# Kernel tuning notes

Hardware: AMD Instinct MI355X
Metric: run time of the kernel (lower is better)

Reference implementation:

```python
import jax, jax.numpy as jnp
import numpy as np

D_MODEL = 1024
D_INNER = 2048   # d_model * expansion_factor(2)
D_CONV = 4
N_EXPERTS = 8
TOP_K = 2


def setup_inputs() -> dict:
    key = jax.random.key(0)
    ks = jax.random.split(key, 6)
    s = 0.02
    return {
        "x": jax.random.normal(ks[0], (4, 2048, D_MODEL), jnp.float32),
        "Wr": jax.random.normal(ks[1], (N_EXPERTS, D_MODEL), jnp.float32) * s,
        "br": jnp.zeros((N_EXPERTS,), jnp.float32),
        "Win": jax.random.normal(ks[2], (N_EXPERTS, 2 * D_INNER, D_MODEL), jnp.float32) * s,
        "conv_w": jax.random.normal(ks[3], (N_EXPERTS, D_INNER, D_CONV), jnp.float32) * s,
        "conv_b": jnp.zeros((N_EXPERTS, D_INNER), jnp.float32),
        "Dp": jnp.ones((N_EXPERTS, D_INNER), jnp.float32),
        "Wout": jax.random.normal(ks[4], (N_EXPERTS, D_MODEL, D_INNER), jnp.float32) * s,
    }


def reference(x, Wr, br, Win, conv_w, conv_b, Dp, Wout):
    B, L, C = x.shape
    xf = x.reshape(-1, C)                                   # [N, C]
    logits = xf @ Wr.T + br                                 # [N, E]
    probs = jax.nn.softmax(logits.astype(jnp.float32), axis=-1)
    tw, ti = jax.lax.top_k(probs, TOP_K)                    # [N, k]
    tw = tw / jnp.sum(tw, axis=-1, keepdims=True)
    oh = jax.nn.one_hot(ti, N_EXPERTS, dtype=jnp.float32)   # [N, k, E]
    load = oh.sum(1).mean(0)                                # [E]
    aux_loss = jnp.sum(load * load)
    # per-token combine weight for each expert (sum over top-k slots)
    cw = jnp.einsum('nk,nke->ne', tw, oh)                   # [N, E]
    out = jnp.zeros_like(xf)
    for j in range(N_EXPERTS):
        # Per-token expert (L=1 inside the original loop): causal depthwise
        # conv with left padding reduces to last-tap * x + bias.
        xz = xf @ Win[j].T                                  # [N, 2*D_INNER]
        xi, z = xz[:, :D_INNER], xz[:, D_INNER:]
        xa = jax.nn.silu(xi * conv_w[j, :, -1] + conv_b[j])
        y = xa * Dp[j] * jax.nn.silu(z)
        out = out + cw[:, j:j + 1].astype(xf.dtype) * (y @ Wout[j].T)
    return out.reshape(B, L, C), aux_loss
```

## Files before the change

### kernel.cpp

```cpp
#include <hip/hip_runtime.h>
#include <hip/hip_bf16.h>
#include <stdint.h>

#define NTOK 8192
#define CDIM 1024
#define DIN  2048
#define NEXP 8
#define NSLOT (NTOK * 2)

typedef __bf16 bf16x8 __attribute__((ext_vector_type(8)));
typedef float  f32x4  __attribute__((ext_vector_type(4)));

typedef __attribute__((address_space(1))) const unsigned char GBUF;
typedef __attribute__((address_space(3))) unsigned char LBUF;

__device__ __forceinline__ void gload_lds16(const void* g, void* l) {
    __builtin_amdgcn_global_load_lds((GBUF*)g, (LBUF*)l, 16, 0, 0);
}

__device__ __forceinline__ ushort f2bf(float f) {
    union { float f; unsigned u; } v; v.f = f;
    unsigned u = v.u;
    u += 0x7fffu + ((u >> 16) & 1u);
    return (ushort)(u >> 16);
}
__device__ __forceinline__ float bf2f(ushort u) {
    union { float f; unsigned u; } v; v.u = ((unsigned)u) << 16; return v.f;
}
__device__ __forceinline__ float silu_f(float x) { return x / (1.f + __expf(-x)); }

__device__ __forceinline__ bf16x8 lds_swz(const ushort* L, int row, int kof) {
    return *(const bf16x8*)&L[row * 64 + ((((kof >> 3) ^ row) & 7) << 3)];
}

__global__ void __launch_bounds__(256) k_cvt(const float* __restrict__ src,
                                             ushort* __restrict__ dst, int n4) {
    int i = blockIdx.x * 256 + threadIdx.x;
    int stride = gridDim.x * 256;
    for (; i < n4; i += stride) {
        float4 v = ((const float4*)src)[i];
        ushort4 o;
        o.x = f2bf(v.x); o.y = f2bf(v.y); o.z = f2bf(v.z); o.w = f2bf(v.w);
        ((ushort4*)dst)[i] = o;
    }
}

__global__ void __launch_bounds__(256) k_router(
    const float* __restrict__ x, const float* __restrict__ Wr,
    const float* __restrict__ br, int* __restrict__ counts,
    int* __restrict__ tok_e, float* __restrict__ tok_w,
    ushort* __restrict__ xb) {
    int wave = blockIdx.x * 4 + (threadIdx.x >> 6);
    int lane = threadIdx.x & 63;
    const float4* row = (const float4*)(x + (size_t)wave * CDIM);
    ushort4* xrow = (ushort4*)(xb + (size_t)wave * CDIM);
    float acc[NEXP];
#pragma unroll
    for (int e = 0; e < NEXP; ++e) acc[e] = 0.f;
#pragma unroll
    for (int j = 0; j < 4; ++j) {
        float4 v = row[j * 64 + lane];
        ushort4 o;
        o.x = f2bf(v.x); o.y = f2bf(v.y); o.z = f2bf(v.z); o.w = f2bf(v.w);
        xrow[j * 64 + lane] = o;
#pragma unroll
        for (int e = 0; e < NEXP; ++e) {
            float4 w = ((const float4*)(Wr + e * CDIM))[j * 64 + lane];
            acc[e] += v.x * w.x + v.y * w.y + v.z * w.z + v.w * w.w;
        }
    }
#pragma unroll
    for (int off = 32; off > 0; off >>= 1)
#pragma unroll
        for (int e = 0; e < NEXP; ++e) acc[e] += __shfl_xor(acc[e], off, 64);
    if (lane == 0) {
        float l[NEXP];
#pragma unroll
        for (int e = 0; e < NEXP; ++e) l[e] = acc[e] + br[e];
        int i0 = 0; float l0 = l[0];
#pragma unroll
        for (int e = 1; e < NEXP; ++e) if (l[e] > l0) { l0 = l[e]; i0 = e; }
        int i1 = -1; float l1 = -1e30f;
#pragma unroll
        for (int e = 0; e < NEXP; ++e) if (e != i0 && l[e] > l1) { l1 = l[e]; i1 = e; }
        float s  = __expf(l1 - l0);
        float w0 = 1.f / (1.f + s);
        float w1 = 1.f - w0;
        tok_e[wave * 2] = i0; tok_e[wave * 2 + 1] = i1;
        tok_w[wave * 2] = w0; tok_w[wave * 2 + 1] = w1;
        atomicAdd(&counts[i0], 1); atomicAdd(&counts[i1], 1);
    }
}

__global__ void k_scan(const int* __restrict__ counts, int* __restrict__ offsets,
                       float* __restrict__ out_aux) {
    if (threadIdx.x == 0 && blockIdx.x == 0) {
        int o = 0;
        for (int e = 0; e < NEXP; ++e) { offsets[e] = o; o += counts[e]; }
        offsets[NEXP] = o;
        float aux = 0.f;
        for (int e = 0; e < NEXP; ++e) {
            float ld = (float)counts[e] * (1.f / (float)NTOK);
            aux += ld * ld;
        }
        *out_aux = aux;
    }
}

__global__ void __launch_bounds__(256) k_scatter(
    const int* __restrict__ tok_e, const float* __restrict__ tok_w,
    const int* __restrict__ offsets, int* __restrict__ cursor,
    int* __restrict__ perm_token, int* __restrict__ tok_slot) {
    int t = blockIdx.x * 256 + threadIdx.x;
    if (t >= NTOK) return;
#pragma unroll
    for (int k = 0; k < 2; ++k) {
        int e = tok_e[t * 2 + k];
        int pos = atomicAdd(&cursor[e], 1);
        int s = offsets[e] + pos;
        perm_token[s] = t;
        tok_slot[t * 2 + k] = s;
    }
}

__global__ void __launch_bounds__(512, 2) k_gemm1(
    const ushort* __restrict__ xb, const ushort* __restrict__ Winb,
    const float* __restrict__ conv_w, const float* __restrict__ conv_b,
    const float* __restrict__ Dp, const int* __restrict__ counts,
    const int* __restrict__ offsets, const int* __restrict__ perm_token,
    ushort* __restrict__ y) {
    int h = blockIdx.x;
    int vb = (h & 7) * 160 + (h >> 3);
    int e   = vb / 160;
    int r   = vb % 160;
    int mt0 = r >> 4;
    int nt  = r & 15;
    int cnt = counts[e];
    if (cnt == 0) return;
    int base = offsets[e];
    int mtiles = (cnt + 255) >> 8;
    int n0 = nt * 128;

    __shared__ ushort aL[2][256 * 64];
    __shared__ ushort bL[2][256 * 64];

    int tid = threadIdx.x, lane = tid & 63, w = tid >> 6;
    int Mw = w >> 1, Nw = w & 1;
    const ushort* WinE = Winb + (size_t)e * (2 * DIN) * CDIM;
    int schunk = ((tid & 7) ^ ((tid >> 3) & 7)) << 3;

    uint bsrc[4];
#pragma unroll
    for (int i = 0; i < 4; ++i) {
        int rr = i * 64 + (tid >> 3);
        int grow = (rr < 128) ? (n0 + rr) : (DIN + n0 + (rr - 128));
        bsrc[i] = (uint)grow * CDIM + schunk;
    }

#define STAGE1(bi, kk0) do { \
        gload_lds16(xb   + asrc[0] + (kk0), &aL[bi][(0 * 512 + tid) * 8]); \
        gload_lds16(xb   + asrc[1] + (kk0), &aL[bi][(1 * 512 + tid) * 8]); \
        gload_lds16(xb   + asrc[2] + (kk0), &aL[bi][(2 * 512 + tid) * 8]); \
        gload_lds16(xb   + asrc[3] + (kk0), &aL[bi][(3 * 512 + tid) * 8]); \
        gload_lds16(WinE + bsrc[0] + (kk0), &bL[bi][(0 * 512 + tid) * 8]); \
        gload_lds16(WinE + bsrc[1] + (kk0), &bL[bi][(1 * 512 + tid) * 8]); \
        gload_lds16(WinE + bsrc[2] + (kk0), &bL[bi][(2 * 512 + tid) * 8]); \
        gload_lds16(WinE + bsrc[3] + (kk0), &bL[bi][(3 * 512 + tid) * 8]); \
    } while (0)

    for (int mt = mt0; mt < mtiles; mt += 10) {
        int rem = cnt - mt * 256;
        uint asrc[4];
#pragma unroll
        for (int i = 0; i < 4; ++i) {
            int rr = i * 64 + (tid >> 3);
            int sidx = base + mt * 256 + (rr < rem ? rr : 0);
            asrc[i] = (uint)perm_token[sidx] * CDIM + schunk;
        }

        f32x4 accXi[4][4], accZ[4][4];
#pragma unroll
        for (int m = 0; m < 4; ++m)
#pragma unroll
            for (int n = 0; n < 4; ++n) {
                accXi[m][n] = f32x4{0.f, 0.f, 0.f, 0.f};
                accZ[m][n]  = f32x4{0.f, 0.f, 0.f, 0.f};
            }

        STAGE1(0, 0);
        __syncthreads();
#pragma unroll 2
        for (int kt = 0; kt < 16; ++kt) {
            int cur = kt & 1;
            if (kt < 15) STAGE1(cur ^ 1, (kt + 1) * 64);
            const ushort* A = &aL[cur][0];
            const ushort* B = &bL[cur][0];
#pragma unroll
            for (int kk = 0; kk < 64; kk += 32) {
                int kof = kk + (lane >> 4) * 8;
                bf16x8 af[4], bxi[4], bz[4];
#pragma unroll
                for (int m = 0; m < 4; ++m)
                    af[m] = lds_swz(A, Mw * 64 + m * 16 + (lane & 15), kof);
#pragma unroll
                for (int n = 0; n < 4; ++n) {
                    int cl = Nw * 64 + n * 16 + (lane & 15);
                    bxi[n] = lds_swz(B, cl, kof);
                    bz[n]  = lds_swz(B, 128 + cl, kof);
                }
#pragma unroll
                for (int m = 0; m < 4; ++m)
#pragma unroll
                    for (int n = 0; n < 4; ++n) {
                        accXi[m][n] = __builtin_amdgcn_mfma_f32_16x16x32_bf16(af[m], bxi[n], accXi[m][n], 0, 0, 0);
                        accZ[m][n]  = __builtin_amdgcn_mfma_f32_16x16x32_bf16(af[m], bz[n],  accZ[m][n],  0, 0, 0);
                    }
            }
            __syncthreads();
        }
#pragma unroll
        for (int n = 0; n < 4; ++n) {
            int c = n0 + Nw * 64 + n * 16 + (lane & 15);
            float cwl = conv_w[((size_t)e * DIN + c) * 4 + 3];
            float cb  = conv_b[(size_t)e * DIN + c];
            float dp  = Dp[(size_t)e * DIN + c];
#pragma unroll
            for (int m = 0; m < 4; ++m)
#pragma unroll
                for (int q = 0; q < 4; ++q) {
                    int rl = Mw * 64 + m * 16 + (lane >> 4) * 4 + q;
                    if (rl < rem) {
                        int slot = base + mt * 256 + rl;
                        float xi = accXi[m][n][q], z = accZ[m][n][q];
                        float yv = silu_f(xi * cwl + cb) * dp * silu_f(z);
                        y[(size_t)slot * DIN + c] = f2bf(yv);
                    }
                }
        }
    }
#undef STAGE1
}

__global__ void __launch_bounds__(512, 2) k_gemm2(
    const ushort* __restrict__ y, const ushort* __restrict__ Woutb,
    const int* __restrict__ counts, const int* __restrict__ offsets,
    ushort* __restrict__ so) {
    int h = blockIdx.x;
    int vb = (h & 7) * 80 + (h >> 3);
    int e   = vb / 80;
    int r   = vb % 80;
    int mt0 = r >> 3;
    int nt  = r & 7;
    int cnt = counts[e];
    if (cnt == 0) return;
    int base = offsets[e];
    int mtiles = (cnt + 255) >> 8;
    int c0 = nt * 128;

    __shared__ ushort aL[2][256 * 64];
    __shared__ ushort bL[2][128 * 64];

    int tid = threadIdx.x, lane = tid & 63, w = tid >> 6;
    int Mw = w >> 1, Nw = w & 1;
    const ushort* WoutE = Woutb + (size_t)e * CDIM * DIN;
    int schunk = ((tid & 7) ^ ((tid >> 3) & 7)) << 3;

    uint bsrc[2];
#pragma unroll
    for (int i = 0; i < 2; ++i) {
        int rr = i * 64 + (tid >> 3);
        bsrc[i] = (uint)(c0 + rr) * DIN + schunk;
    }

#define STAGE2(bi, kk0) do { \
        gload_lds16(y     + asrc[0] + (kk0), &aL[bi][(0 * 512 + tid) * 8]); \
        gload_lds16(y     + asrc[1] + (kk0), &aL[bi][(1 * 512 + tid) * 8]); \
        gload_lds16(y     + asrc[2] + (kk0), &aL[bi][(2 * 512 + tid) * 8]); \
        gload_lds16(y     + asrc[3] + (kk0), &aL[bi][(3 * 512 + tid) * 8]); \
        gload_lds16(WoutE + bsrc[0] + (kk0), &bL[bi][(0 * 512 + tid) * 8]); \
        gload_lds16(WoutE + bsrc[1] + (kk0), &bL[bi][(1 * 512 + tid) * 8]); \
    } while (0)

    for (int mt = mt0; mt < mtiles; mt += 10) {
        int rem = cnt - mt * 256;
        uint asrc[4];
#pragma unroll
        for (int i = 0; i < 4; ++i) {
            int rr = i * 64 + (tid >> 3);
            int slot = base + mt * 256 + (rr < rem ? rr : 0);
            asrc[i] = (uint)slot * DIN + schunk;
        }
        f32x4 acc[4][4];
#pragma unroll
        for (int m = 0; m < 4; ++m)
#pragma unroll
            for (int n = 0; n < 4; ++n) acc[m][n] = f32x4{0.f, 0.f, 0.f, 0.f};

        STAGE2(0, 0);
        __syncthreads();
#pragma unroll 2
        for (int kt = 0; kt < 32; ++kt) {
            int cur = kt & 1;
            if (kt < 31) STAGE2(cur ^ 1, (kt + 1) * 64);
            const ushort* A = &aL[cur][0];
            const ushort* B = &bL[cur][0];
#pragma unroll
            for (int kk = 0; kk < 64; kk += 32) {
                int kof = kk + (lane >> 4) * 8;
                bf16x8 af[4], bfr[4];
#pragma unroll
                for (int m = 0; m < 4; ++m)
                    af[m] = lds_swz(A, Mw * 64 + m * 16 + (lane & 15), kof);
#pragma unroll
                for (int n = 0; n < 4; ++n)
                    bfr[n] = lds_swz(B, Nw * 64 + n * 16 + (lane & 15), kof);
#pragma unroll
                for (int m = 0; m < 4; ++m)
#pragma unroll
                    for (int n = 0; n < 4; ++n)
                        acc[m][n] = __builtin_amdgcn_mfma_f32_16x16x32_bf16(af[m], bfr[n], acc[m][n], 0, 0, 0);
            }
            __syncthreads();
        }
#pragma unroll
        for (int m = 0; m < 4; ++m)
#pragma unroll
            for (int q = 0; q < 4; ++q) {
                int rl = Mw * 64 + m * 16 + (lane >> 4) * 4 + q;
                if (rl < rem) {
                    int slot = base + mt * 256 + rl;
#pragma unroll
                    for (int n = 0; n < 4; ++n) {
                        int col = c0 + Nw * 64 + n * 16 + (lane & 15);
                        so[(size_t)slot * CDIM + col] = f2bf(acc[m][n][q]);
                    }
                }
            }
    }
#undef STAGE2
}

__global__ void __launch_bounds__(256) k_combine(
    const ushort* __restrict__ so, const int* __restrict__ tok_slot,
    const float* __restrict__ tok_w, float* __restrict__ out) {
    int i = blockIdx.x * 256 + threadIdx.x;
    int t  = i >> 7;
    int c8 = (i & 127) << 3;
    int s0 = tok_slot[t * 2], s1 = tok_slot[t * 2 + 1];
    float w0 = tok_w[t * 2],  w1 = tok_w[t * 2 + 1];
    uint4 a = *(const uint4*)(so + (size_t)s0 * CDIM + c8);
    uint4 b = *(const uint4*)(so + (size_t)s1 * CDIM + c8);
    const ushort* au = (const ushort*)&a;
    const ushort* bu = (const ushort*)&b;
    float4 o0, o1;
    o0.x = w0 * bf2f(au[0]) + w1 * bf2f(bu[0]);
    o0.y = w0 * bf2f(au[1]) + w1 * bf2f(bu[1]);
    o0.z = w0 * bf2f(au[2]) + w1 * bf2f(bu[2]);
    o0.w = w0 * bf2f(au[3]) + w1 * bf2f(bu[3]);
    o1.x = w0 * bf2f(au[4]) + w1 * bf2f(bu[4]);
    o1.y = w0 * bf2f(au[5]) + w1 * bf2f(bu[5]);
    o1.z = w0 * bf2f(au[6]) + w1 * bf2f(bu[6]);
    o1.w = w0 * bf2f(au[7]) + w1 * bf2f(bu[7]);
    float4* dst = (float4*)(out + (size_t)t * CDIM + c8);
    dst[0] = o0; dst[1] = o1;
}

extern "C" void kernel_launch(void* const* d_in, const int* in_sizes, int n_in,
                              void* d_out, int out_size, void* d_ws, size_t ws_size,
                              hipStream_t stream) {
    const float* x      = (const float*)d_in[0];
    const float* Wr     = (const float*)d_in[1];
    const float* br     = (const float*)d_in[2];
    const float* Win    = (const float*)d_in[3];
    const float* conv_w = (const float*)d_in[4];
    const float* conv_b = (const float*)d_in[5];
    const float* Dp     = (const float*)d_in[6];
    const float* Wout   = (const float*)d_in[7];
    float* out = (float*)d_out;

    char* ws = (char*)d_ws;
    int*    counts     = (int*)(ws + 0);
    int*    offsets    = (int*)(ws + 64);
    int*    cursor     = (int*)(ws + 128);
    int*    tok_e      = (int*)(ws + 4096);
    float*  tok_w      = (float*)(ws + 4096 + 1 * 65536);
    int*    perm_token = (int*)(ws + 4096 + 2 * 65536);
    int*    tok_slot   = (int*)(ws + 4096 + 3 * 65536);
    const size_t MB = 1u << 20;
    ushort* y     = (ushort*)(ws + MB);
    ushort* xb    = (ushort*)(ws + MB + 67108864);
    ushort* winb  = (ushort*)(ws + MB + 67108864 + 16777216);
    ushort* woutb = (ushort*)(ws + MB + 67108864 + 16777216 + 67108864);
    ushort* so    = winb;

    hipMemsetAsync(ws, 0, 256, stream);

    k_cvt<<<2048, 256, 0, stream>>>(Win,  winb,  NEXP * 2 * DIN * CDIM / 4);
    k_cvt<<<1024, 256, 0, stream>>>(Wout, woutb, NEXP * CDIM * DIN / 4);

    k_router<<<NTOK / 4, 256, 0, stream>>>(x, Wr, br, counts, tok_e, tok_w, xb);
    k_scan<<<1, 64, 0, stream>>>(counts, offsets, out + (size_t)NTOK * CDIM);
    k_scatter<<<NTOK / 256, 256, 0, stream>>>(tok_e, tok_w, offsets, cursor, perm_token, tok_slot);

    k_gemm1<<<NEXP * 160, 512, 0, stream>>>(xb, winb, conv_w, conv_b, Dp,
                                            counts, offsets, perm_token, y);
    k_gemm2<<<NEXP * 80, 512, 0, stream>>>(y, woutb, counts, offsets, so);
    k_combine<<<NTOK * 128 / 256, 256, 0, stream>>>(so, tok_slot, tok_w, out);
}
```

Before: 631.3 us.

## Pipeline GEMM K-loops with partial vmcnt waits and explicit barriers

Restructures the double-buffered K loops in both expert GEMMs. Each loop now issues the next stage's global-to-LDS loads and then waits only for the previous stage using s_waitcnt vmcnt(N) and raw s_barrier, instead of __syncthreads, which drains every outstanding load. The intent is to keep the next tile's loads in flight while MFMAs run on the current tile. It also raises wave priority around the MFMA section with s_setprio. The risk is that the hand-chosen vmcnt counts must exactly match the number of loads each STAGE issues, or LDS reads could race with incoming data.

```diff
diff --git a/kernel.cpp b/kernel.cpp
--- a/kernel.cpp
+++ b/kernel.cpp
@@ -32,6 +32,10 @@
 __device__ __forceinline__ bf16x8 lds_swz(const ushort* L, int row, int kof) {
     return *(const bf16x8*)&L[row * 64 + ((((kof >> 3) ^ row) & 7) << 3)];
 }
+
+#define WAITV(N) do { asm volatile("s_waitcnt vmcnt(" #N ")" ::: "memory"); \
+                      __builtin_amdgcn_sched_barrier(0); } while (0)
+#define BARR     __builtin_amdgcn_s_barrier()
 
 __global__ void __launch_bounds__(256) k_cvt(const float* __restrict__ src,
                                              ushort* __restrict__ dst, int n4) {
@@ -187,14 +191,8 @@
                 accZ[m][n]  = f32x4{0.f, 0.f, 0.f, 0.f};
             }
 
-        STAGE1(0, 0);
-        __syncthreads();
-#pragma unroll 2
-        for (int kt = 0; kt < 16; ++kt) {
-            int cur = kt & 1;
-            if (kt < 15) STAGE1(cur ^ 1, (kt + 1) * 64);
-            const ushort* A = &aL[cur][0];
-            const ushort* B = &bL[cur][0];
+        auto compute = [&](const ushort* A, const ushort* B) {
+            __builtin_amdgcn_s_setprio(1);
 #pragma unroll
             for (int kk = 0; kk < 64; kk += 32) {
                 int kof = kk + (lane >> 4) * 8;
@@ -216,8 +214,28 @@
                         accZ[m][n]  = __builtin_amdgcn_mfma_f32_16x16x32_bf16(af[m], bz[n],  accZ[m][n],  0, 0, 0);
                     }
             }
-            __syncthreads();
-        }
+            __builtin_amdgcn_s_setprio(0);
+        };
+
+        STAGE1(0, 0);
+#pragma unroll 1
+        for (int kt = 0; kt + 2 <= 15; kt += 2) {
+            STAGE1(1, (kt + 1) * 64);
+            WAITV(8); BARR;
+            compute(&aL[0][0], &bL[0][0]);
+            BARR;
+            STAGE1(0, (kt + 2) * 64);
+            WAITV(8); BARR;
+            compute(&aL[1][0], &bL[1][0]);
+            BARR;
+        }
+        STAGE1(1, 15 * 64);
+        WAITV(8); BARR;
+        compute(&aL[0][0], &bL[0][0]);
+        BARR;
+        WAITV(0); BARR;
+        compute(&aL[1][0], &bL[1][0]);
+
 #pragma unroll
         for (int n = 0; n < 4; ++n) {
             int c = n0 + Nw * 64 + n * 16 + (lane & 15);
@@ -237,6 +255,7 @@
                     }
                 }
         }
+        BARR;
     }
 #undef STAGE1
 }
@@ -296,14 +315,8 @@
 #pragma unroll
             for (int n = 0; n < 4; ++n) acc[m][n] = f32x4{0.f, 0.f, 0.f, 0.f};
 
-        STAGE2(0, 0);
-        __syncthreads();
-#pragma unroll 2
-        for (int kt = 0; kt < 32; ++kt) {
-            int cur = kt & 1;
-            if (kt < 31) STAGE2(cur ^ 1, (kt + 1) * 64);
-            const ushort* A = &aL[cur][0];
-            const ushort* B = &bL[cur][0];
+        auto compute = [&](const ushort* A, const ushort* B) {
+            __builtin_amdgcn_s_setprio(1);
 #pragma unroll
             for (int kk = 0; kk < 64; kk += 32) {
                 int kof = kk + (lane >> 4) * 8;
@@ -320,8 +333,28 @@
                     for (int n = 0; n < 4; ++n)
                         acc[m][n] = __builtin_amdgcn_mfma_f32_16x16x32_bf16(af[m], bfr[n], acc[m][n], 0, 0, 0);
             }
-            __syncthreads();
-        }
+            __builtin_amdgcn_s_setprio(0);
+        };
+
+        STAGE2(0, 0);
+#pragma unroll 1
+        for (int kt = 0; kt + 2 <= 31; kt += 2) {
+            STAGE2(1, (kt + 1) * 64);
+            WAITV(6); BARR;
+            compute(&aL[0][0], &bL[0][0]);
+            BARR;
+            STAGE2(0, (kt + 2) * 64);
+            WAITV(6); BARR;
+            compute(&aL[1][0], &bL[1][0]);
+            BARR;
+        }
+        STAGE2(1, 31 * 64);
+        WAITV(6); BARR;
+        compute(&aL[0][0], &bL[0][0]);
+        BARR;
+        WAITV(0); BARR;
+        compute(&aL[1][0], &bL[1][0]);
+
 #pragma unroll
         for (int m = 0; m < 4; ++m)
 #pragma unroll
@@ -336,6 +369,7 @@
                     }
                 }
             }
+        BARR;
     }
 #undef STAGE2
 }
```

After: 656.1 us. 1.04x slower.
